# Optimization experiments

Hardware: AMD Instinct MI355X
Metric: run time of the kernel (lower is better)

## Reference

```python
import jax, jax.numpy as jnp
from jax import lax
import numpy as np

B, N, C = 16, 8192, 256


def farthest_point_sample(pts, npoint):
    # pts: [B, N, 3]. Standard PointNet++ FPS; is_center=True -> start from the
    # point farthest from the centroid (argmax of dist-to-mean).
    b, n, _ = pts.shape
    centroid = pts.mean(axis=1, keepdims=True)                  # [B,1,3]
    d0 = jnp.sum((pts - centroid) ** 2, axis=-1)                # [B,N]
    farthest = jnp.argmax(d0, axis=-1)                          # [B]
    dist = jnp.full((b, n), 1e10, dtype=pts.dtype)

    def step(carry, _):
        dist, far = carry
        cur = jnp.take_along_axis(pts, far[:, None, None], axis=1)  # [B,1,3]
        d = jnp.sum((pts - cur) ** 2, axis=-1)                      # [B,N]
        dist = jnp.minimum(dist, d)
        new_far = jnp.argmax(dist, axis=-1)
        return (dist, new_far), far

    (_, _), idxs = lax.scan(step, (dist, farthest), None, length=npoint)
    return idxs.T  # [B, npoint]


def index_points(x, idx):
    # x: [B, N, D], idx: [B, M] -> [B, M, D]
    return jnp.take_along_axis(x, idx[:, :, None], axis=1)


def setup_inputs() -> dict:
    key = jax.random.key(0)
    k1, k2 = jax.random.split(key)
    points = jax.random.normal(k1, (B, 3, N), dtype=jnp.float32)
    features = jax.random.normal(k2, (B, C, N), dtype=jnp.float32)
    return {"points": points, "features": features, "num_points": 2048}


def reference(points, features, num_points):
    pts = jnp.swapaxes(points, -1, -2)     # [B,N,3]
    feats = jnp.swapaxes(features, -1, -2) # [B,N,C]
    idx = farthest_point_sample(pts, num_points)  # [B,M] int
    sampled_points = index_points(pts, idx)       # [B,M,3]
    sampled_features = index_points(feats, idx)   # [B,M,C]
    return sampled_points, sampled_features
```

## Files before the change

### kernel.cpp

```cpp
#include <hip/hip_runtime.h>
#include <cfloat>

#define BB 16
#define NN 8192
#define CC 256
#define NT 512
#define PPT 16
#define NPAIR (PPT / 2)
#define NWAVES (NT / 64)
#define TBLOCKS 240
#define NTILES (BB * (CC / 64) * (NN / 64))

typedef float v2f __attribute__((ext_vector_type(2)));

struct SmemFPS {
  float4 p4[NN];
  unsigned long long key[2][NWAVES];
  float red[NWAVES][3];
  float ctr[3];
};
struct SmemT {
  float tile[64][65];
};
union Smem { SmemFPS f; SmemT t; };

__device__ __forceinline__ unsigned long long max64(unsigned long long a,
                                                    unsigned long long b) {
  return a > b ? a : b;
}

template <int CTRL>
__device__ __forceinline__ unsigned long long dpp_max64(unsigned long long x) {
  int lo = (int)(unsigned)x;
  int hi = (int)(unsigned)(x >> 32);
  int plo = __builtin_amdgcn_update_dpp(0, lo, CTRL, 0xF, 0xF, true);
  int phi = __builtin_amdgcn_update_dpp(0, hi, CTRL, 0xF, 0xF, true);
  unsigned long long p =
      ((unsigned long long)(unsigned)phi << 32) | (unsigned)plo;
  return max64(x, p);
}

__device__ __forceinline__ unsigned long long wave_max63(unsigned long long k) {
  k = dpp_max64<0xB1>(k);
  k = dpp_max64<0x4E>(k);
  k = dpp_max64<0x124>(k);
  k = dpp_max64<0x128>(k);
  k = dpp_max64<0x142>(k);
  k = dpp_max64<0x143>(k);
  return k;
}

__global__ __launch_bounds__(NT)
void fps_fused_kernel(const float* __restrict__ pts,
                      const float* __restrict__ feats,
                      float* __restrict__ out_pts,
                      int* __restrict__ idx_out,
                      float* __restrict__ trans, int M, int do_trans) {
  __shared__ Smem sm;
  const int t = threadIdx.x;

  if (blockIdx.x >= BB) {
    if (!do_trans) return;
    for (int tileId = blockIdx.x - BB; tileId < NTILES; tileId += TBLOCKS) {
      int b  = tileId / ((CC / 64) * (NN / 64));
      int r  = tileId % ((CC / 64) * (NN / 64));
      int ct = r / (NN / 64);
      int nt = r % (NN / 64);
      const float* src = feats + ((size_t)b * CC + ct * 64) * NN + nt * 64;
      float* dst = trans + ((size_t)b * NN + nt * 64) * CC + ct * 64;
#pragma unroll
      for (int i = 0; i < 2; ++i) {
        int f = t + i * NT;
        int c = f >> 4, n4 = f & 15;
        float4 v = *(const float4*)(src + (size_t)c * NN + n4 * 4);
        sm.t.tile[c][n4 * 4 + 0] = v.x;
        sm.t.tile[c][n4 * 4 + 1] = v.y;
        sm.t.tile[c][n4 * 4 + 2] = v.z;
        sm.t.tile[c][n4 * 4 + 3] = v.w;
      }
      __syncthreads();
#pragma unroll
      for (int i = 0; i < 2; ++i) {
        int f = t + i * NT;
        int n = f >> 4, c4 = f & 15;
        float4 o;
        o.x = sm.t.tile[c4 * 4 + 0][n];
        o.y = sm.t.tile[c4 * 4 + 1][n];
        o.z = sm.t.tile[c4 * 4 + 2][n];
        o.w = sm.t.tile[c4 * 4 + 3][n];
        *(float4*)(dst + (size_t)n * CC + c4 * 4) = o;
      }
      __syncthreads();
    }
    return;
  }

  const int b = blockIdx.x;
  const int wave = t >> 6;
  const int lane = t & 63;
  const float* base = pts + (size_t)b * 3 * NN;

  v2f px2[NPAIR], py2[NPAIR], pz2[NPAIR], dist2[NPAIR];
#pragma unroll
  for (int j = 0; j < NPAIR; ++j) {
    int n0 = t + (2 * j) * NT;
    int n1 = t + (2 * j + 1) * NT;
    float x0 = base[n0], y0 = base[NN + n0], z0 = base[2 * NN + n0];
    float x1 = base[n1], y1 = base[NN + n1], z1 = base[2 * NN + n1];
    px2[j] = (v2f){x0, x1};
    py2[j] = (v2f){y0, y1};
    pz2[j] = (v2f){z0, z1};
    sm.f.p4[n0] = make_float4(x0, y0, z0, 0.f);
    sm.f.p4[n1] = make_float4(x1, y1, z1, 0.f);
    dist2[j] = (v2f){1e10f, 1e10f};
  }

  float sx = 0.f, sy = 0.f, sz = 0.f;
#pragma unroll
  for (int j = 0; j < NPAIR; ++j) {
    sx += px2[j].x; sx += px2[j].y;
    sy += py2[j].x; sy += py2[j].y;
    sz += pz2[j].x; sz += pz2[j].y;
  }
#pragma unroll
  for (int off = 32; off > 0; off >>= 1) {
    sx += __shfl_xor(sx, off);
    sy += __shfl_xor(sy, off);
    sz += __shfl_xor(sz, off);
  }
  if (lane == 0) { sm.f.red[wave][0] = sx; sm.f.red[wave][1] = sy; sm.f.red[wave][2] = sz; }
  __syncthreads();
  if (t == 0) {
    float gx = 0.f, gy = 0.f, gz = 0.f;
    for (int w = 0; w < NWAVES; ++w) { gx += sm.f.red[w][0]; gy += sm.f.red[w][1]; gz += sm.f.red[w][2]; }
    sm.f.ctr[0] = gx / NN; sm.f.ctr[1] = gy / NN; sm.f.ctr[2] = gz / NN;
  }
  __syncthreads();
  const float ctx = sm.f.ctr[0], cty = sm.f.ctr[1], ctz = sm.f.ctr[2];

  int ep = 0;
  int ci;

  auto reduce_tail = [&](float v, int bk) {
    unsigned long long key =
        ((unsigned long long)__float_as_uint(v) << 32) |
        (unsigned)(~(t + bk * NT));
    key = wave_max63(key);
    ep ^= 1;
    if (lane == 63) sm.f.key[ep][wave] = key;
    __syncthreads();
    unsigned long long k0 = max64(sm.f.key[ep][0], sm.f.key[ep][1]);
    unsigned long long k1 = max64(sm.f.key[ep][2], sm.f.key[ep][3]);
    unsigned long long k2 = max64(sm.f.key[ep][4], sm.f.key[ep][5]);
    unsigned long long k3 = max64(sm.f.key[ep][6], sm.f.key[ep][7]);
    ci = (int)~(unsigned)max64(max64(k0, k1), max64(k2, k3));
  };

  {
    v2f c2x = {ctx, ctx}, c2y = {cty, cty}, c2z = {ctz, ctz};
    v2f nd2[NPAIR];
    float v = -FLT_MAX;
    {
#pragma clang fp contract(off)
#pragma unroll
      for (int j = 0; j < NPAIR; ++j) {
        v2f dx = px2[j] - c2x, dy = py2[j] - c2y, dz = pz2[j] - c2z;
        v2f d = (dx * dx + dy * dy) + dz * dz;
        nd2[j] = d;
        v = fmaxf(fmaxf(v, d.x), d.y);
      }
    }
    int bk = 0;
#pragma unroll
    for (int k = PPT - 1; k >= 0; --k) {
      float ndk = (k & 1) ? nd2[k >> 1].y : nd2[k >> 1].x;
      if (ndk == v) bk = k;
    }
    reduce_tail(v, bk);
  }

  for (int m = 0; m < M; ++m) {
    float4 c4 = sm.f.p4[ci];
    if (t == 0) {
      idx_out[b * M + m] = ci;
      size_t o = ((size_t)b * M + m) * 3;
      out_pts[o] = c4.x; out_pts[o + 1] = c4.y; out_pts[o + 2] = c4.z;
    }
    if (m == M - 1) break;

    v2f c2x = {c4.x, c4.x}, c2y = {c4.y, c4.y}, c2z = {c4.z, c4.z};
    v2f nd2[NPAIR];
    float v = -FLT_MAX;
    {
#pragma clang fp contract(off)
#pragma unroll
      for (int j = 0; j < NPAIR; ++j) {
        v2f dx = px2[j] - c2x, dy = py2[j] - c2y, dz = pz2[j] - c2z;
        v2f d = (dx * dx + dy * dy) + dz * dz;
        v2f nd;
        nd.x = fminf(dist2[j].x, d.x);
        nd.y = fminf(dist2[j].y, d.y);
        dist2[j] = nd;
        nd2[j] = nd;
        v = fmaxf(fmaxf(v, nd.x), nd.y);
      }
    }
    int bk = 0;
#pragma unroll
    for (int k = PPT - 1; k >= 0; --k) {
      float ndk = (k & 1) ? nd2[k >> 1].y : nd2[k >> 1].x;
      if (ndk == v) bk = k;
    }
    reduce_tail(v, bk);
  }
}

__global__ __launch_bounds__(256)
void gather_t_kernel(const float* __restrict__ trans,
                     const int* __restrict__ idx,
                     float* __restrict__ out_f, int M) {
  int gm = blockIdx.x * 4 + (threadIdx.x >> 6);
  if (gm >= BB * M) return;
  int lane = threadIdx.x & 63;
  int b = gm / M;
  int n = idx[gm];
  float4 v = *(const float4*)(trans + ((size_t)b * NN + n) * CC + lane * 4);
  *(float4*)(out_f + (size_t)gm * CC + lane * 4) = v;
}

__global__ __launch_bounds__(CC)
void gather_kernel(const float* __restrict__ feats, const int* __restrict__ idx,
                   float* __restrict__ out_f, int M) {
  const int bm = blockIdx.x;
  const int b = bm / M;
  const int n = idx[bm];
  const int c = threadIdx.x;
  out_f[(size_t)bm * CC + c] = feats[((size_t)b * CC + c) * NN + n];
}

extern "C" void kernel_launch(void* const* d_in, const int* in_sizes, int n_in,
                              void* d_out, int out_size, void* d_ws, size_t ws_size,
                              hipStream_t stream) {
  const float* points = (const float*)d_in[0];
  const float* feats  = (const float*)d_in[1];
  int M = out_size / (BB * (3 + CC));
  if (M <= 0) M = 1;

  float* out_pts = (float*)d_out;
  float* out_f   = (float*)d_out + (size_t)BB * M * 3;

  int* idx_ws = (int*)d_ws;
  size_t idx_bytes = (((size_t)BB * M * sizeof(int)) + 255) & ~(size_t)255;
  size_t trans_bytes = (size_t)BB * NN * CC * sizeof(float);
  bool use_t = (ws_size >= idx_bytes + trans_bytes);
  float* trans = (float*)((char*)d_ws + idx_bytes);

  int grid = use_t ? (BB + TBLOCKS) : BB;
  fps_fused_kernel<<<dim3(grid), dim3(NT), 0, stream>>>(
      points, feats, out_pts, idx_ws, trans, M, use_t ? 1 : 0);

  if (use_t) {
    gather_t_kernel<<<dim3((BB * M + 3) / 4), dim3(256), 0, stream>>>(
        trans, idx_ws, out_f, M);
  } else {
    gather_kernel<<<dim3(BB * M), dim3(CC), 0, stream>>>(feats, idx_ws, out_f, M);
  }
}
```

Measured before the change: 2.244 ms.

## Use packed-FP32 inline asm, integer min/max on distances, and DPP cross-wave reduce

```diff
diff --git a/kernel.cpp b/kernel.cpp
--- a/kernel.cpp
+++ b/kernel.cpp
@@ -11,11 +11,14 @@
 #define TBLOCKS 240
 #define NTILES (BB * (CC / 64) * (NN / 64))
 
-typedef float v2f __attribute__((ext_vector_type(2)));
+typedef float    v2f __attribute__((ext_vector_type(2)));
+typedef unsigned v2u __attribute__((ext_vector_type(2)));
+typedef unsigned uu;
+typedef unsigned long long ull;
 
 struct SmemFPS {
-  float4 p4[NN];
-  unsigned long long key[2][NWAVES];
+  float px[NN], py[NN], pz[NN];
+  ull   key[2][NWAVES];
   float red[NWAVES][3];
   float ctr[3];
 };
@@ -24,23 +27,39 @@
 };
 union Smem { SmemFPS f; SmemT t; };
 
-__device__ __forceinline__ unsigned long long max64(unsigned long long a,
-                                                    unsigned long long b) {
-  return a > b ? a : b;
-}
+__device__ __forceinline__ v2f pk_sub(v2f a, v2f b) {
+  v2f d;
+  asm("v_pk_add_f32 %0, %1, %2 neg_lo:[0,1] neg_hi:[0,1]"
+      : "=v"(d) : "v"(a), "v"(b));
+  return d;
+}
+__device__ __forceinline__ v2f pk_mul(v2f a, v2f b) {
+  v2f d;
+  asm("v_pk_mul_f32 %0, %1, %2" : "=v"(d) : "v"(a), "v"(b));
+  return d;
+}
+__device__ __forceinline__ v2f pk_add(v2f a, v2f b) {
+  v2f d;
+  asm("v_pk_add_f32 %0, %1, %2" : "=v"(d) : "v"(a), "v"(b));
+  return d;
+}
+
+__device__ __forceinline__ uu umin2(uu a, uu b) { return a < b ? a : b; }
+__device__ __forceinline__ uu umax2(uu a, uu b) { return a > b ? a : b; }
+
+__device__ __forceinline__ ull max64(ull a, ull b) { return a > b ? a : b; }
 
 template <int CTRL>
-__device__ __forceinline__ unsigned long long dpp_max64(unsigned long long x) {
-  int lo = (int)(unsigned)x;
-  int hi = (int)(unsigned)(x >> 32);
+__device__ __forceinline__ ull dpp_max64(ull x) {
+  int lo = (int)(uu)x;
+  int hi = (int)(uu)(x >> 32);
   int plo = __builtin_amdgcn_update_dpp(0, lo, CTRL, 0xF, 0xF, true);
   int phi = __builtin_amdgcn_update_dpp(0, hi, CTRL, 0xF, 0xF, true);
-  unsigned long long p =
-      ((unsigned long long)(unsigned)phi << 32) | (unsigned)plo;
+  ull p = ((ull)(uu)phi << 32) | (uu)plo;
   return max64(x, p);
 }
 
-__device__ __forceinline__ unsigned long long wave_max63(unsigned long long k) {
+__device__ __forceinline__ ull wave_max63(ull k) {
   k = dpp_max64<0xB1>(k);
   k = dpp_max64<0x4E>(k);
   k = dpp_max64<0x124>(k);
@@ -100,7 +119,9 @@
   const int lane = t & 63;
   const float* base = pts + (size_t)b * 3 * NN;
 
-  v2f px2[NPAIR], py2[NPAIR], pz2[NPAIR], dist2[NPAIR];
+  v2f px2[NPAIR], py2[NPAIR], pz2[NPAIR];
+  v2u dist2[NPAIR];
+  const uu INIT = __float_as_uint(1e10f);
 #pragma unroll
   for (int j = 0; j < NPAIR; ++j) {
     int n0 = t + (2 * j) * NT;
@@ -110,9 +131,9 @@
     px2[j] = (v2f){x0, x1};
     py2[j] = (v2f){y0, y1};
     pz2[j] = (v2f){z0, z1};
-    sm.f.p4[n0] = make_float4(x0, y0, z0, 0.f);
-    sm.f.p4[n1] = make_float4(x1, y1, z1, 0.f);
-    dist2[j] = (v2f){1e10f, 1e10f};
+    sm.f.px[n0] = x0; sm.f.py[n0] = y0; sm.f.pz[n0] = z0;
+    sm.f.px[n1] = x1; sm.f.py[n1] = y1; sm.f.pz[n1] = z1;
+    dist2[j] = (v2u){INIT, INIT};
   }
 
   float sx = 0.f, sy = 0.f, sz = 0.f;
@@ -141,74 +162,71 @@
   int ep = 0;
   int ci;
 
-  auto reduce_tail = [&](float v, int bk) {
-    unsigned long long key =
-        ((unsigned long long)__float_as_uint(v) << 32) |
-        (unsigned)(~(t + bk * NT));
+  auto reduce_tail = [&](uu v, int bk) {
+    ull key = ((ull)v << 32) | (uu)(~(t + (bk << 9)));
     key = wave_max63(key);
     ep ^= 1;
     if (lane == 63) sm.f.key[ep][wave] = key;
     __syncthreads();
-    unsigned long long k0 = max64(sm.f.key[ep][0], sm.f.key[ep][1]);
-    unsigned long long k1 = max64(sm.f.key[ep][2], sm.f.key[ep][3]);
-    unsigned long long k2 = max64(sm.f.key[ep][4], sm.f.key[ep][5]);
-    unsigned long long k3 = max64(sm.f.key[ep][6], sm.f.key[ep][7]);
-    ci = (int)~(unsigned)max64(max64(k0, k1), max64(k2, k3));
+    ull kk = sm.f.key[ep][lane & 7];
+    kk = dpp_max64<0xB1>(kk);
+    kk = dpp_max64<0x4E>(kk);
+    kk = dpp_max64<0x124>(kk);
+    ci = (int)~(uu)kk;
   };
 
   {
     v2f c2x = {ctx, ctx}, c2y = {cty, cty}, c2z = {ctz, ctz};
-    v2f nd2[NPAIR];
-    float v = -FLT_MAX;
-    {
-#pragma clang fp contract(off)
-#pragma unroll
-      for (int j = 0; j < NPAIR; ++j) {
-        v2f dx = px2[j] - c2x, dy = py2[j] - c2y, dz = pz2[j] - c2z;
-        v2f d = (dx * dx + dy * dy) + dz * dz;
-        nd2[j] = d;
-        v = fmaxf(fmaxf(v, d.x), d.y);
-      }
+    v2u nd2[NPAIR];
+    uu v = 0u;
+#pragma unroll
+    for (int j = 0; j < NPAIR; ++j) {
+      v2f dx = pk_sub(px2[j], c2x);
+      v2f dy = pk_sub(py2[j], c2y);
+      v2f dz = pk_sub(pz2[j], c2z);
+      v2f d = pk_add(pk_add(pk_mul(dx, dx), pk_mul(dy, dy)), pk_mul(dz, dz));
+      v2u du = (v2u){__float_as_uint(d.x), __float_as_uint(d.y)};
+      nd2[j] = du;
+      v = umax2(v, umax2(du.x, du.y));
     }
     int bk = 0;
 #pragma unroll
     for (int k = PPT - 1; k >= 0; --k) {
-      float ndk = (k & 1) ? nd2[k >> 1].y : nd2[k >> 1].x;
+      uu ndk = (k & 1) ? nd2[k >> 1].y : nd2[k >> 1].x;
       if (ndk == v) bk = k;
     }
     reduce_tail(v, bk);
   }
 
   for (int m = 0; m < M; ++m) {
-    float4 c4 = sm.f.p4[ci];
+    float cx = sm.f.px[ci], cy = sm.f.py[ci], cz = sm.f.pz[ci];
     if (t == 0) {
       idx_out[b * M + m] = ci;
       size_t o = ((size_t)b * M + m) * 3;
-      out_pts[o] = c4.x; out_pts[o + 1] = c4.y; out_pts[o + 2] = c4.z;
+      out_pts[o] = cx; out_pts[o + 1] = cy; out_pts[o + 2] = cz;
     }
     if (m == M - 1) break;
 
-    v2f c2x = {c4.x, c4.x}, c2y = {c4.y, c4.y}, c2z = {c4.z, c4.z};
-    v2f nd2[NPAIR];
-    float v = -FLT_MAX;
-    {
-#pragma clang fp contract(off)
-#pragma unroll
-      for (int j = 0; j < NPAIR; ++j) {
-        v2f dx = px2[j] - c2x, dy = py2[j] - c2y, dz = pz2[j] - c2z;
-        v2f d = (dx * dx + dy * dy) + dz * dz;
-        v2f nd;
-        nd.x = fminf(dist2[j].x, d.x);
-        nd.y = fminf(dist2[j].y, d.y);
-        dist2[j] = nd;
-        nd2[j] = nd;
-        v = fmaxf(fmaxf(v, nd.x), nd.y);
-      }
+    v2f c2x = {cx, cx}, c2y = {cy, cy}, c2z = {cz, cz};
+    v2u nd2[NPAIR];
+    uu v = 0u;
+#pragma unroll
+    for (int j = 0; j < NPAIR; ++j) {
+      v2f dx = pk_sub(px2[j], c2x);
+      v2f dy = pk_sub(py2[j], c2y);
+      v2f dz = pk_sub(pz2[j], c2z);
+      v2f d = pk_add(pk_add(pk_mul(dx, dx), pk_mul(dy, dy)), pk_mul(dz, dz));
+      v2u nd;
+      nd.x = umin2(dist2[j].x, __float_as_uint(d.x));
+      nd.y = umin2(dist2[j].y, __float_as_uint(d.y));
+      dist2[j] = nd;
+      nd2[j] = nd;
+      v = umax2(v, umax2(nd.x, nd.y));
     }
     int bk = 0;
 #pragma unroll
     for (int k = PPT - 1; k >= 0; --k) {
-      float ndk = (k & 1) ? nd2[k >> 1].y : nd2[k >> 1].x;
+      uu ndk = (k & 1) ? nd2[k >> 1].y : nd2[k >> 1].x;
       if (ndk == v) bk = k;
     }
     reduce_tail(v, bk);
```

New measurement: 1.945 ms. 13.3% less time.
